# Kernel optimization log

Measured on AMD Instinct MI355X. Metric: run time of the kernel, lower is better.

Reference implementation:

```python
import jax, jax.numpy as jnp
import numpy as np

N_HEADS = 16
ROPE_THETA = 10000.0


def _rope_cos_sin(seq_len, head_dim):
    # freqs for pairs (2i, 2i+1): [seq_len, head_dim//2]
    inv_freq = 1.0 / (ROPE_THETA ** (jnp.arange(0, head_dim, 2, dtype=jnp.float32) / head_dim))
    angles = jnp.arange(seq_len, dtype=jnp.float32)[:, None] * inv_freq[None, :]
    return jnp.cos(angles), jnp.sin(angles)


def _apply_rope(t, cos, sin):
    # t: [B, H, S, hd]; complex multiply on interleaved pairs
    tr = t.reshape(*t.shape[:-1], -1, 2)  # [B,H,S,hd//2,2]
    x0, x1 = tr[..., 0], tr[..., 1]
    r0 = x0 * cos - x1 * sin
    r1 = x0 * sin + x1 * cos
    return jnp.stack([r0, r1], axis=-1).reshape(t.shape)


def setup_inputs() -> dict:
    key = jax.random.key(0)
    ks = jax.random.split(key, 5)
    B, S, D = 2, 2048, 2048
    scale = 0.02
    return {
        "x": jax.random.normal(ks[0], (B, S, D), jnp.float32),
        "wq": jax.random.normal(ks[1], (D, D), jnp.float32) * scale,
        "wk": jax.random.normal(ks[2], (D, D), jnp.float32) * scale,
        "wv": jax.random.normal(ks[3], (D, D), jnp.float32) * scale,
        "wo": jax.random.normal(ks[4], (D, D), jnp.float32) * scale,
    }


def reference(x, wq, wk, wv, wo):
    B, S, D = x.shape
    H = N_HEADS
    hd = D // H
    # QKV projections (Linear with no bias: x @ W.T), split heads -> [B,H,S,hd]
    def proj(w):
        return jnp.einsum('bsd,ed->bse', x, w).reshape(B, S, H, hd).transpose(0, 2, 1, 3)
    q, k, v = proj(wq), proj(wk), proj(wv)
    cos, sin = _rope_cos_sin(S, hd)  # [S, hd//2] each
    cos = cos[None, None]            # [1,1,S,hd//2]
    sin = sin[None, None]
    q = _apply_rope(q, cos, sin)
    k = _apply_rope(k, cos, sin)
    # causal SDPA
    scores = jnp.einsum('bhqd,bhkd->bhqk', q, k) / jnp.sqrt(jnp.float32(hd))
    causal = jnp.tril(jnp.ones((S, S), dtype=bool))
    scores = jnp.where(causal, scores, jnp.finfo(scores.dtype).min)
    attn = jax.nn.softmax(scores, axis=-1)
    out = jnp.einsum('bhqk,bhkd->bhqd', attn, v)
    out = out.transpose(0, 2, 1, 3).reshape(B, S, D)
    return jnp.einsum('bsd,ed->bse', out, wo)
```

## Files before the change

kernel.cpp:

```cpp
#include <hip/hip_runtime.h>
#include <stdint.h>

typedef __attribute__((ext_vector_type(4))) float f32x4;
typedef __attribute__((ext_vector_type(8))) short short8;
typedef __attribute__((ext_vector_type(4))) short s16x4;

#define DEV __device__ __forceinline__

constexpr int Bc = 2, Sc = 2048, Dc = 2048, Hc = 16, HDc = 128;
constexpr int Mc = Bc * Sc;
constexpr float ATTN_SCALE = 0.08838834764831843f;

DEV short f2bf(float f) {
  unsigned u = __float_as_uint(f);
  unsigned r = (u + 0x7fffu + ((u >> 16) & 1u)) >> 16;
  return (short)(unsigned short)r;
}

DEV void gload_lds16(const void* gsrc, void* ldst) {
  typedef const __attribute__((address_space(1))) void as1_cvoid;
  typedef __attribute__((address_space(3))) void as3_void;
  __builtin_amdgcn_global_load_lds((as1_cvoid*)(uintptr_t)gsrc,
                                   (as3_void*)(uint32_t)(uintptr_t)ldst,
                                   16, 0, 0);
}

__global__ void cast_f32_bf16(const float* __restrict__ in, short* __restrict__ out, int n8) {
  int i = blockIdx.x * 256 + threadIdx.x;
  if (i >= n8) return;
  f32x4 a = ((const f32x4*)in)[i * 2];
  f32x4 b = ((const f32x4*)in)[i * 2 + 1];
  short8 o;
  o[0] = f2bf(a[0]); o[1] = f2bf(a[1]); o[2] = f2bf(a[2]); o[3] = f2bf(a[3]);
  o[4] = f2bf(b[0]); o[5] = f2bf(b[1]); o[6] = f2bf(b[2]); o[7] = f2bf(b[3]);
  ((short8*)out)[i] = o;
}

__global__ void rope_table(float* __restrict__ ct, float* __restrict__ st) {
  int t = blockIdx.x * 256 + threadIdx.x;
  int s = t >> 6, i = t & 63;
  float freq = powf(10000.0f, -(float)(2 * i) * (1.0f / 128.0f));
  float a = (float)s * freq;
  float sv, cv;
  sincosf(a, &sv, &cv);
  ct[t] = cv; st[t] = sv;
}

template <int EPI>
__global__ __launch_bounds__(512, 2) void gemm_pipe(
    const short* __restrict__ A,
    const short* __restrict__ W0, const short* __restrict__ W1, const short* __restrict__ W2,
    short* __restrict__ qo, short* __restrict__ ko, short* __restrict__ vo,
    float* __restrict__ outf,
    const float* __restrict__ ct, const float* __restrict__ st) {
  constexpr int K = Dc, NT = K / 64;
  __shared__ short As[2][128][64];
  __shared__ short Bs[2][2][128][64];

  const int tid = threadIdx.x, lane = tid & 63, w = tid >> 6;
  const int g = lane >> 4, c = lane & 15;
  const int wr = w >> 2, wc = w & 3;

  const int nx = gridDim.x;
  const int nwg = nx * gridDim.y;
  const int flat = blockIdx.y * nx + blockIdx.x;
  const int swz = (flat & 7) * (nwg >> 3) + (flat >> 3);
  const int nbx = swz % nx, nby = swz / nx;

  const int m0 = nby * 128;
  const int which = (EPI == 0) ? (nbx >> 3) : 0;
  const int wn0 = (EPI == 0) ? ((nbx & 7) * 256) : (nbx * 256);
  const short* W = (EPI == 1) ? W0 : ((which == 0) ? W0 : (which == 1) ? W1 : W2);

  const int r1 = tid >> 3, p1 = tid & 7;
  const int psw = (p1 ^ (r1 & 7)) * 8;
  const short* gA0 = A + (size_t)(m0 + r1) * K + psw;
  const short* gA1 = gA0 + (size_t)64 * K;
  const short* gB0 = W + (size_t)(wn0 + r1) * K + psw;
  const short* gB1 = gB0 + (size_t)64 * K;
  const short* gB2 = gB0 + (size_t)128 * K;
  const short* gB3 = gB0 + (size_t)192 * K;
  char* ldsA = (char*)As + w * 1024;
  char* ldsB = (char*)Bs + w * 1024;

#define STAGE(t, db)                                        \
  do {                                                      \
    const size_t ko_ = (size_t)(t) * 64;                    \
    gload_lds16(gA0 + ko_, ldsA + (db) * 16384);            \
    gload_lds16(gA1 + ko_, ldsA + (db) * 16384 + 8192);     \
    gload_lds16(gB0 + ko_, ldsB + (db) * 32768);            \
    gload_lds16(gB1 + ko_, ldsB + (db) * 32768 + 8192);     \
    gload_lds16(gB2 + ko_, ldsB + (db) * 32768 + 16384);    \
    gload_lds16(gB3 + ko_, ldsB + (db) * 32768 + 24576);    \
  } while (0)

  f32x4 acc[4][4] = {};
  const int cx = (g ^ (c & 7)) * 16;
  const char* aBase = (const char*)As + (wr * 64 + c) * 128;
  const char* bBase = (const char*)Bs + (wc >> 1) * 16384 + ((wc & 1) * 64 + c) * 128;

  STAGE(0, 0);
  STAGE(1, 1);
  asm volatile("s_waitcnt vmcnt(6)" ::: "memory");
  __builtin_amdgcn_sched_barrier(0);
  __builtin_amdgcn_s_barrier();

  for (int t = 0; t < NT; ++t) {
    const int db = t & 1;
    short8 af[2][4], bf[2][4];
    const char* aB = aBase + db * 16384;
    const char* bB = bBase + db * 32768;
#pragma unroll
    for (int kk = 0; kk < 2; ++kk) {
      const int co = cx ^ (kk * 64);
#pragma unroll
      for (int mi = 0; mi < 4; ++mi) af[kk][mi] = *(const short8*)(aB + mi * 2048 + co);
#pragma unroll
      for (int nj = 0; nj < 4; ++nj) bf[kk][nj] = *(const short8*)(bB + nj * 2048 + co);
    }
    asm volatile("s_waitcnt lgkmcnt(0)" ::: "memory");
    __builtin_amdgcn_sched_barrier(0);
    __builtin_amdgcn_s_barrier();
    __builtin_amdgcn_sched_barrier(0);
    if (t + 2 < NT) STAGE(t + 2, db);
    __builtin_amdgcn_s_setprio(1);
#pragma unroll
    for (int kk = 0; kk < 2; ++kk)
#pragma unroll
      for (int mi = 0; mi < 4; ++mi)
#pragma unroll
        for (int nj = 0; nj < 4; ++nj)
          acc[mi][nj] = __builtin_amdgcn_mfma_f32_16x16x32_bf16(af[kk][mi], bf[kk][nj], acc[mi][nj], 0, 0, 0);
    __builtin_amdgcn_s_setprio(0);
    if (t + 2 < NT) { asm volatile("s_waitcnt vmcnt(6)" ::: "memory"); }
    else            { asm volatile("s_waitcnt vmcnt(0)" ::: "memory"); }
    __builtin_amdgcn_sched_barrier(0);
    __builtin_amdgcn_s_barrier();
  }
#undef STAGE

  if constexpr (EPI == 0) {
    if (which < 2) {
      short* outb = (which == 0) ? qo : ko;
#pragma unroll
      for (int mi = 0; mi < 4; ++mi)
#pragma unroll
        for (int nj = 0; nj < 4; ++nj)
#pragma unroll
          for (int r = 0; r < 4; ++r) {
            int row = m0 + wr * 64 + mi * 16 + g * 4 + r;
            int col = wn0 + wc * 64 + nj * 16 + c;
            float v = acc[mi][nj][r];
            float other = __shfl_xor(v, 1);
            int pi = (col & (HDc - 1)) >> 1;
            int sp = row & (Sc - 1);
            float cv = ct[sp * 64 + pi], sv = st[sp * 64 + pi];
            v = ((col & 1) == 0) ? (v * cv - other * sv) : (other * sv + v * cv);
            int b_ = row >> 11, sq = row & (Sc - 1);
            int h_ = col >> 7, dd = col & (HDc - 1);
            outb[((size_t)(b_ * Hc + h_) * Sc + sq) * HDc + dd] = f2bf(v);
          }
    } else {
#pragma unroll
      for (int mi = 0; mi < 4; ++mi)
#pragma unroll
        for (int nj = 0; nj < 4; ++nj) {
          int row0 = m0 + wr * 64 + mi * 16 + g * 4;
          int col = wn0 + wc * 64 + nj * 16 + c;
          int b_ = row0 >> 11, sq0 = row0 & (Sc - 1);
          int h_ = col >> 7, dd = col & (HDc - 1);
          s16x4 pk;
#pragma unroll
          for (int r = 0; r < 4; ++r) pk[r] = f2bf(acc[mi][nj][r]);
          *(s16x4*)&vo[((size_t)(b_ * Hc + h_) * HDc + dd) * Sc + sq0] = pk;
        }
    }
  } else {
#pragma unroll
    for (int mi = 0; mi < 4; ++mi)
#pragma unroll
      for (int nj = 0; nj < 4; ++nj)
#pragma unroll
        for (int r = 0; r < 4; ++r) {
          int row = m0 + wr * 64 + mi * 16 + g * 4 + r;
          int col = wn0 + wc * 64 + nj * 16 + c;
          outf[(size_t)row * Dc + col] = acc[mi][nj][r];
        }
  }
}

DEV void stage_kv(const short* kh, const short* vth, int kv0,
                  short* Kb, short* Vb, int w, int tid) {
#pragma unroll
  for (int i = 0; i < 4; ++i) {
    int L = i * 256 + tid;
    int row = L >> 4, p = L & 15;
    gload_lds16(kh + (size_t)(kv0 + row) * HDc + ((p ^ (row & 7)) * 8),
                (char*)Kb + i * 4096 + w * 1024);
  }
#pragma unroll
  for (int i = 0; i < 4; ++i) {
    int L = i * 256 + tid;
    int row = L >> 3, p = L & 7;
    gload_lds16(vth + (size_t)row * Sc + kv0 + ((p ^ (row & 7)) * 8),
                (char*)Vb + i * 4096 + w * 1024);
  }
}

__global__ __launch_bounds__(256) void attn_kernel(
    const short* __restrict__ qb, const short* __restrict__ kb,
    const short* __restrict__ vtb, short* __restrict__ ob) {
  __shared__ short Kl[2][64 * 128];
  __shared__ short Vl[2][128 * 64];
  __shared__ short Pl[4 * 16 * 72];

  const int tid = threadIdx.x, lane = tid & 63, w = tid >> 6;
  const int g = lane >> 4, c = lane & 15;
  const int bh = blockIdx.y;
  const int b_ = bh >> 4, h_ = bh & 15;
  const short* qh = qb + (size_t)bh * Sc * HDc;
  const short* kh = kb + (size_t)bh * Sc * HDc;
  const short* vth = vtb + (size_t)bh * HDc * Sc;

  for (int pass = 0; pass < 2; ++pass) {
    const int qt = pass ? (31 - blockIdx.x) : blockIdx.x;
    const int q0 = qt * 64;

    short8 qf[4];
#pragma unroll
    for (int kc = 0; kc < 4; ++kc)
      qf[kc] = *(const short8*)&qh[(size_t)(q0 + w * 16 + c) * HDc + kc * 32 + g * 8];

    float mrow[4], lrow[4];
    f32x4 acc[8] = {};
#pragma unroll
    for (int r = 0; r < 4; ++r) { mrow[r] = -1e30f; lrow[r] = 0.f; }

    const int nt = qt + 1;
    int cur = 0;
    stage_kv(kh, vth, 0, Kl[0], Vl[0], w, tid);
    __syncthreads();

    for (int kvt = 0; kvt < nt; ++kvt) {
      if (kvt + 1 < nt)
        stage_kv(kh, vth, (kvt + 1) * 64, Kl[cur ^ 1], Vl[cur ^ 1], w, tid);

      f32x4 sacc[4];
#pragma unroll
      for (int kb_ = 0; kb_ < 4; ++kb_) {
        sacc[kb_] = (f32x4){0.f, 0.f, 0.f, 0.f};
#pragma unroll
        for (int kc = 0; kc < 4; ++kc) {
          short8 kf = *(const short8*)&Kl[cur][(kb_ * 16 + c) * 128 + (((kc * 4 + g) ^ (c & 7)) * 8)];
          sacc[kb_] = __builtin_amdgcn_mfma_f32_16x16x32_bf16(qf[kc], kf, sacc[kb_], 0, 0, 0);
        }
      }
      float p[4][4];
      const bool last = (kvt == qt);
      const int kv0 = kvt * 64;
#pragma unroll
      for (int kb_ = 0; kb_ < 4; ++kb_)
#pragma unroll
        for (int r = 0; r < 4; ++r) {
          float s = sacc[kb_][r] * ATTN_SCALE;
          if (last) {
            int qg = q0 + w * 16 + g * 4 + r;
            int kg = kv0 + kb_ * 16 + c;
            if (kg > qg) s = -1e30f;
          }
          p[kb_][r] = s;
        }
      float scal[4];
#pragma unroll
      for (int r = 0; r < 4; ++r) {
        float v = fmaxf(fmaxf(p[0][r], p[1][r]), fmaxf(p[2][r], p[3][r]));
        v = fmaxf(v, __shfl_xor(v, 1));
        v = fmaxf(v, __shfl_xor(v, 2));
        v = fmaxf(v, __shfl_xor(v, 4));
        v = fmaxf(v, __shfl_xor(v, 8));
        float mn = fmaxf(mrow[r], v);
        scal[r] = __expf(mrow[r] - mn);
        mrow[r] = mn;
      }
#pragma unroll
      for (int r = 0; r < 4; ++r) {
        float acc_s = 0.f;
#pragma unroll
        for (int kb_ = 0; kb_ < 4; ++kb_) {
          p[kb_][r] = __expf(p[kb_][r] - mrow[r]);
          acc_s += p[kb_][r];
        }
        acc_s += __shfl_xor(acc_s, 1);
        acc_s += __shfl_xor(acc_s, 2);
        acc_s += __shfl_xor(acc_s, 4);
        acc_s += __shfl_xor(acc_s, 8);
        lrow[r] = lrow[r] * scal[r] + acc_s;
      }
#pragma unroll
      for (int db = 0; db < 8; ++db)
#pragma unroll
        for (int r = 0; r < 4; ++r) acc[db][r] *= scal[r];
#pragma unroll
      for (int kb_ = 0; kb_ < 4; ++kb_)
#pragma unroll
        for (int r = 0; r < 4; ++r)
          Pl[w * 16 * 72 + (g * 4 + r) * 72 + kb_ * 16 + c] = f2bf(p[kb_][r]);
      short8 pa[2];
#pragma unroll
      for (int k2 = 0; k2 < 2; ++k2)
        pa[k2] = *(const short8*)&Pl[w * 16 * 72 + c * 72 + k2 * 32 + g * 8];
#pragma unroll
      for (int db = 0; db < 8; ++db)
#pragma unroll
        for (int k2 = 0; k2 < 2; ++k2) {
          short8 vf = *(const short8*)&Vl[cur][(db * 16 + c) * 64 + (((k2 * 4 + g) ^ (c & 7)) * 8)];
          acc[db] = __builtin_amdgcn_mfma_f32_16x16x32_bf16(pa[k2], vf, acc[db], 0, 0, 0);
        }
      __syncthreads();
      cur ^= 1;
    }

#pragma unroll
    for (int db = 0; db < 8; ++db)
#pragma unroll
      for (int r = 0; r < 4; ++r) {
        int qg = q0 + w * 16 + g * 4 + r;
        int d = db * 16 + c;
        float v = acc[db][r] / lrow[r];
        ob[((size_t)(b_ * Sc + qg)) * Dc + h_ * HDc + d] = f2bf(v);
      }
  }
}

extern "C" void kernel_launch(void* const* d_in, const int* in_sizes, int n_in,
                              void* d_out, int out_size, void* d_ws, size_t ws_size,
                              hipStream_t stream) {
  const float* x = (const float*)d_in[0];
  const float* wq = (const float*)d_in[1];
  const float* wk = (const float*)d_in[2];
  const float* wv = (const float*)d_in[3];
  const float* wo = (const float*)d_in[4];
  float* out = (float*)d_out;

  char* ws = (char*)d_ws;
  short* xb  = (short*)(ws + 0);
  short* wqb = (short*)(ws + 16777216);
  short* wkb = (short*)(ws + 25165824);
  short* wvb = (short*)(ws + 33554432);
  short* wob = (short*)(ws + 41943040);
  short* qb  = (short*)(ws + 50331648);
  short* kbf = (short*)(ws + 67108864);
  short* vtb = (short*)(ws + 83886080);
  float* ct  = (float*)(ws + 100663296);
  float* st  = (float*)(ws + 101187584);
  short* obuf = xb;

  cast_f32_bf16<<<Mc * Dc / 8 / 256, 256, 0, stream>>>(x, xb, Mc * Dc / 8);
  cast_f32_bf16<<<Dc * Dc / 8 / 256, 256, 0, stream>>>(wq, wqb, Dc * Dc / 8);
  cast_f32_bf16<<<Dc * Dc / 8 / 256, 256, 0, stream>>>(wk, wkb, Dc * Dc / 8);
  cast_f32_bf16<<<Dc * Dc / 8 / 256, 256, 0, stream>>>(wv, wvb, Dc * Dc / 8);
  cast_f32_bf16<<<Dc * Dc / 8 / 256, 256, 0, stream>>>(wo, wob, Dc * Dc / 8);
  rope_table<<<Sc * 64 / 256, 256, 0, stream>>>(ct, st);

  gemm_pipe<0><<<dim3(24, 32), 512, 0, stream>>>(xb, wqb, wkb, wvb, qb, kbf, vtb, nullptr, ct, st);

  attn_kernel<<<dim3(Sc / 128, Bc * Hc), 256, 0, stream>>>(qb, kbf, vtb, obuf);

  gemm_pipe<1><<<dim3(8, 32), 512, 0, stream>>>(obuf, wob, nullptr, nullptr,
                                                nullptr, nullptr, nullptr, out, ct, st);
}
```

Measured before the change: 397.1 us.

## Double-buffer register fragments to overlap LDS reads with MFMA in GEMM loop

New measurement: 392.4 us. About the same (-1.2%).

```diff
diff --git a/kernel.cpp b/kernel.cpp
--- a/kernel.cpp
+++ b/kernel.cpp
@@ -99,45 +99,73 @@
   const char* aBase = (const char*)As + (wr * 64 + c) * 128;
   const char* bBase = (const char*)Bs + (wc >> 1) * 16384 + ((wc & 1) * 64 + c) * 128;
 
+  short8 afA[2][4], bfA[2][4], afB[2][4], bfB[2][4];
+
+#define READ_FRAGS(af, bf, db)                                                        \
+  do {                                                                                \
+    const char* aB = aBase + (db) * 16384;                                            \
+    const char* bB = bBase + (db) * 32768;                                            \
+    _Pragma("unroll")                                                                 \
+    for (int kk = 0; kk < 2; ++kk) {                                                  \
+      const int co = cx ^ (kk * 64);                                                  \
+      _Pragma("unroll")                                                               \
+      for (int mi = 0; mi < 4; ++mi) af[kk][mi] = *(const short8*)(aB + mi * 2048 + co); \
+      _Pragma("unroll")                                                               \
+      for (int nj = 0; nj < 4; ++nj) bf[kk][nj] = *(const short8*)(bB + nj * 2048 + co); \
+    }                                                                                 \
+  } while (0)
+
+#define MFMA_ALL(af, bf)                                                              \
+  do {                                                                                \
+    _Pragma("unroll")                                                                 \
+    for (int kk = 0; kk < 2; ++kk)                                                    \
+      _Pragma("unroll")                                                               \
+      for (int mi = 0; mi < 4; ++mi)                                                  \
+        _Pragma("unroll")                                                             \
+        for (int nj = 0; nj < 4; ++nj)                                                \
+          acc[mi][nj] = __builtin_amdgcn_mfma_f32_16x16x32_bf16(af[kk][mi], bf[kk][nj], acc[mi][nj], 0, 0, 0); \
+  } while (0)
+
   STAGE(0, 0);
   STAGE(1, 1);
   asm volatile("s_waitcnt vmcnt(6)" ::: "memory");
   __builtin_amdgcn_sched_barrier(0);
   __builtin_amdgcn_s_barrier();
-
-  for (int t = 0; t < NT; ++t) {
-    const int db = t & 1;
-    short8 af[2][4], bf[2][4];
-    const char* aB = aBase + db * 16384;
-    const char* bB = bBase + db * 32768;
-#pragma unroll
-    for (int kk = 0; kk < 2; ++kk) {
-      const int co = cx ^ (kk * 64);
-#pragma unroll
-      for (int mi = 0; mi < 4; ++mi) af[kk][mi] = *(const short8*)(aB + mi * 2048 + co);
-#pragma unroll
-      for (int nj = 0; nj < 4; ++nj) bf[kk][nj] = *(const short8*)(bB + nj * 2048 + co);
-    }
+  READ_FRAGS(afA, bfA, 0);
+  asm volatile("s_waitcnt lgkmcnt(0)" ::: "memory");
+  __builtin_amdgcn_sched_barrier(0);
+  __builtin_amdgcn_s_barrier();
+
+  for (int t = 0; t < NT; t += 2) {
+    if (t + 2 < NT) { STAGE(t + 2, 0); asm volatile("s_waitcnt vmcnt(6)" ::: "memory"); }
+    else            { asm volatile("s_waitcnt vmcnt(0)" ::: "memory"); }
+    __builtin_amdgcn_sched_barrier(0);
+    __builtin_amdgcn_s_barrier();
+    READ_FRAGS(afB, bfB, 1);
+    __builtin_amdgcn_sched_barrier(0);
+    __builtin_amdgcn_s_setprio(1);
+    MFMA_ALL(afA, bfA);
+    __builtin_amdgcn_s_setprio(0);
     asm volatile("s_waitcnt lgkmcnt(0)" ::: "memory");
     __builtin_amdgcn_sched_barrier(0);
     __builtin_amdgcn_s_barrier();
-    __builtin_amdgcn_sched_barrier(0);
-    if (t + 2 < NT) STAGE(t + 2, db);
+
+    if (t + 3 < NT) { STAGE(t + 3, 1); asm volatile("s_waitcnt vmcnt(6)" ::: "memory"); }
+    else            { asm volatile("s_waitcnt vmcnt(0)" ::: "memory"); }
+    __builtin_amdgcn_sched_barrier(0);
+    __builtin_amdgcn_s_barrier();
+    if (t + 2 < NT) READ_FRAGS(afA, bfA, 0);
+    __builtin_amdgcn_sched_barrier(0);
     __builtin_amdgcn_s_setprio(1);
-#pragma unroll
-    for (int kk = 0; kk < 2; ++kk)
-#pragma unroll
-      for (int mi = 0; mi < 4; ++mi)
-#pragma unroll
-        for (int nj = 0; nj < 4; ++nj)
-          acc[mi][nj] = __builtin_amdgcn_mfma_f32_16x16x32_bf16(af[kk][mi], bf[kk][nj], acc[mi][nj], 0, 0, 0);
+    MFMA_ALL(afB, bfB);
     __builtin_amdgcn_s_setprio(0);
-    if (t + 2 < NT) { asm volatile("s_waitcnt vmcnt(6)" ::: "memory"); }
-    else            { asm volatile("s_waitcnt vmcnt(0)" ::: "memory"); }
+    asm volatile("s_waitcnt lgkmcnt(0)" ::: "memory");
     __builtin_amdgcn_sched_barrier(0);
     __builtin_amdgcn_s_barrier();
   }
 #undef STAGE
+#undef READ_FRAGS
+#undef MFMA_ALL
 
   if constexpr (EPI == 0) {
     if (which < 2) {
```
